# Performance work log

Hardware: AMD Instinct MI355X
Metric: run time of the kernel (lower is better)

The kernel has to match this reference:

```python
import jax, jax.numpy as jnp
import numpy as np

K = 16  # centroids per codebook (4-bit LUT indices, blink-mm convention)


def _im2col(x, kh, kw, stride, pad):
    # x: [B, C, H, W] -> [B, P, C*kh*kw] with channel-major feature ordering
    # (each length-(kh*kw) subvector is one channel's patch, matching the
    #  per-channel codebook layout of the 3x3 AMM conv).
    B, C, H, W = x.shape
    xp = jnp.pad(x, ((0, 0), (0, 0), (pad, pad), (pad, pad)))
    Ho = (H + 2 * pad - kh) // stride + 1
    Wo = (W + 2 * pad - kw) // stride + 1
    cols = [xp[:, :, i:i + stride * Ho:stride, j:j + stride * Wo:stride]
            for i in range(kh) for j in range(kw)]  # fixed small loop (<=9)
    feat = jnp.stack(cols, axis=2)                      # [B, C, kh*kw, Ho, Wo]
    feat = feat.reshape(B, C * kh * kw, Ho, Wo)
    feat = feat.transpose(0, 2, 3, 1).reshape(B, Ho * Wo, C * kh * kw)
    return feat, Ho, Wo


def _amm_conv_bn_act(x, centroids, lut, scale, bias, kernel, stride, pad, relu):
    # Product-quantization approximate matmul conv:
    #  1) im2col, split feature dim D into ncodebooks subspaces of dim dsub
    #  2) nearest-centroid (L2) assignment per subspace -> 4-bit index
    #  3) gather+accumulate precomputed LUT dot products over codebooks
    #  4) folded BatchNorm affine + optional ReLU
    feat, Ho, Wo = _im2col(x, kernel, kernel, stride, pad)
    B, P, D = feat.shape
    ncb, k, dsub = centroids.shape
    xs = feat.reshape(B, P, ncb, dsub)
    dots = jnp.einsum('bpcd,ckd->bpck', xs, centroids)          # [B,P,ncb,K]
    c2 = jnp.sum(centroids * centroids, axis=-1)                # [ncb,K]
    idx = jnp.argmin(c2[None, None] - 2.0 * dots, axis=-1)      # [B,P,ncb]
    onehot = jax.nn.one_hot(idx, k, dtype=x.dtype)              # [B,P,ncb,K]
    out = jnp.einsum('bpck,cko->bpo', onehot, lut)              # LUT accumulate
    out = out * scale + bias                                    # folded BN
    if relu:
        out = jax.nn.relu(out)
    Cout = lut.shape[-1]
    return out.reshape(B, Ho, Wo, Cout).transpose(0, 3, 1, 2)


def setup_inputs() -> dict:
    key = jax.random.key(0)
    ks = jax.random.split(key, 16)
    inplanes, planes, width = 1024, 256, 256
    B, H, W = 32, 14, 14
    d = {}
    d['x'] = jax.random.normal(ks[0], (B, inplanes, H, W), dtype=jnp.float32)
    d['c1_centroids'] = jax.random.normal(ks[1], (inplanes // 4, K, 4), dtype=jnp.float32)
    d['c1_lut'] = jax.random.normal(ks[2], (inplanes // 4, K, width), dtype=jnp.float32) * 0.1
    d['c1_scale'] = jax.random.uniform(ks[3], (width,), dtype=jnp.float32, minval=0.5, maxval=1.5)
    d['c1_bias'] = jax.random.normal(ks[4], (width,), dtype=jnp.float32) * 0.1
    d['c2_centroids'] = jax.random.normal(ks[5], (width, K, 9), dtype=jnp.float32)
    d['c2_lut'] = jax.random.normal(ks[6], (width, K, width), dtype=jnp.float32) * 0.1
    d['c2_scale'] = jax.random.uniform(ks[7], (width,), dtype=jnp.float32, minval=0.5, maxval=1.5)
    d['c2_bias'] = jax.random.normal(ks[8], (width,), dtype=jnp.float32) * 0.1
    d['c3_centroids'] = jax.random.normal(ks[9], (width // 4, K, 4), dtype=jnp.float32)
    d['c3_lut'] = jax.random.normal(ks[10], (width // 4, K, planes * 4), dtype=jnp.float32) * 0.1
    d['c3_scale'] = jax.random.uniform(ks[11], (planes * 4,), dtype=jnp.float32, minval=0.5, maxval=1.5)
    d['c3_bias'] = jax.random.normal(ks[12], (planes * 4,), dtype=jnp.float32) * 0.1
    return d


def reference(x, c1_centroids, c1_lut, c1_scale, c1_bias,
              c2_centroids, c2_lut, c2_scale, c2_bias,
              c3_centroids, c3_lut, c3_scale, c3_bias):
    identity = x
    out = _amm_conv_bn_act(x, c1_centroids, c1_lut, c1_scale, c1_bias,
                           kernel=1, stride=1, pad=0, relu=True)
    out = _amm_conv_bn_act(out, c2_centroids, c2_lut, c2_scale, c2_bias,
                           kernel=3, stride=1, pad=1, relu=True)
    out = _amm_conv_bn_act(out, c3_centroids, c3_lut, c3_scale, c3_bias,
                           kernel=1, stride=1, pad=0, relu=False)
    # QuantizedAdd + QuantizedReLU (float reference math: add then relu)
    return jax.nn.relu(out + identity)
```

## Files before the change

kernel.cpp:

```cpp
#include <hip/hip_runtime.h>
#include <stdint.h>

#define PP 196
#define BP 6272

typedef _Float16 half_t;
typedef half_t half8v __attribute__((ext_vector_type(8)));
typedef half_t half2v __attribute__((ext_vector_type(2)));


template <typename T>
__global__ __launch_bounds__(256) void assign_1x1(
    const T* __restrict__ in, const float* __restrict__ cents,
    uint32_t* __restrict__ idxp, int nchan) {
  __shared__ float  sf[8][16][4];
  __shared__ double sd[8][16][6];
  const int chunk = blockIdx.y;
  const int t = threadIdx.x;
  for (int i = t; i < 512; i += 256) {
    float c = cents[(size_t)chunk * 512 + i];
    int cb = i >> 6, r = i & 63;
    sf[cb][r >> 2][r & 3] = c;
    sd[cb][r >> 2][1 + (r & 3)] = (double)c;
  }
  __syncthreads();
  if (t < 128) {
    int cb = t >> 4, k = t & 15;
    double s = 0.0;
#pragma unroll
    for (int d = 0; d < 4; d++) { double c = sd[cb][k][1 + d]; s += c * c; }
    sd[cb][k][0] = s;
  }
  __syncthreads();
  const int p = blockIdx.x * 256 + t;
  if (p >= BP) return;
  const unsigned b = (unsigned)p / 196u;
  const unsigned pr = (unsigned)p - b * 196u;
  const T* xb = in + ((size_t)b * nchan + chunk * 32) * PP + pr;
  T xr[32];
#pragma unroll
  for (int i = 0; i < 32; i++) xr[i] = xb[(size_t)i * PP];
  float xs2[32];
#pragma unroll
  for (int i = 0; i < 32; i++) xs2[i] = 2.f * (float)xr[i];
  uint32_t word = 0;
#pragma unroll 1
  for (int cb = 0; cb < 8; cb++) {
    float best = 1e30f, sec = 1e30f; int bi = 0;
#pragma unroll
    for (int k = 0; k < 16; k++) {
      const float4 c = *(const float4*)&sf[cb][k][0];
      float dist = c.x * (c.x - xs2[cb * 4 + 0]);
      dist = fmaf(c.y, c.y - xs2[cb * 4 + 1], dist);
      dist = fmaf(c.z, c.z - xs2[cb * 4 + 2], dist);
      dist = fmaf(c.w, c.w - xs2[cb * 4 + 3], dist);
      if (dist < best) { sec = best; best = dist; bi = k; }
      else sec = fminf(sec, dist);
    }
    if (__any(sec - best < 2e-4f)) {
      double xv[4];
#pragma unroll
      for (int d = 0; d < 4; d++) xv[d] = (double)xr[cb * 4 + d];
      double bb = 1e300; int bi64 = 0;
#pragma unroll
      for (int k = 0; k < 16; k++) {
        double dot = 0.0;
#pragma unroll
        for (int d = 0; d < 4; d++) dot = fma(xv[d], sd[cb][k][1 + d], dot);
        double dist = sd[cb][k][0] - 2.0 * dot;
        if (dist < bb) { bb = dist; bi64 = k; }
      }
      bi = bi64;
    }
    word |= (uint32_t)bi << (4 * cb);
  }
  idxp[(size_t)chunk * BP + p] = word;
}

__global__ __launch_bounds__(256) void assign_3x3(
    const double* __restrict__ in, const float* __restrict__ cents,
    uint32_t* __restrict__ idxp) {
  __shared__ float  sf[8][16][12];
  __shared__ double sd[8][16][10];
  const int chunk = blockIdx.y;
  const int c0g = chunk * 8;
  const int t = threadIdx.x;
  for (int i = t; i < 1152; i += 256) {
    int cb = i / 144, r = i - cb * 144;
    int k = r / 9, d = r - k * 9;
    float c = cents[(size_t)(c0g + cb) * 144 + k * 9 + d];
    sf[cb][k][1 + d] = c;
    sd[cb][k][1 + d] = (double)c;
  }
  __syncthreads();
  if (t < 128) {
    int cb = t >> 4, k = t & 15;
    double s = 0.0;
    float s32 = 0.f;
#pragma unroll
    for (int d = 0; d < 9; d++) {
      double c = sd[cb][k][1 + d]; s += c * c;
      float cf = sf[cb][k][1 + d]; s32 += cf * cf;
    }
    sd[cb][k][0] = s;
    sf[cb][k][0] = s32;
  }
  __syncthreads();
  const int p = blockIdx.x * 256 + t;
  if (p >= BP) return;
  const unsigned b = (unsigned)p / 196u;
  const unsigned pr = (unsigned)p - b * 196u;
  const int oh = pr / 14, ow = pr - oh * 14;
  uint32_t word = 0;
#pragma unroll 1
  for (int cb = 0; cb < 8; cb++) {
    const double* base = in + ((size_t)b * 256 + (c0g + cb)) * PP;
    double v64[9]; float v32[9];
#pragma unroll
    for (int r = 0; r < 3; r++) {
#pragma unroll
      for (int cc = 0; cc < 3; cc++) {
        int hh = oh + r - 1, ww = ow + cc - 1;
        bool ok = (hh >= 0) & (hh < 14) & (ww >= 0) & (ww < 14);
        double v = ok ? base[hh * 14 + ww] : 0.0;
        v64[r * 3 + cc] = v;
        v32[r * 3 + cc] = (float)v;
      }
    }
    float best = 1e30f, sec = 1e30f; int bi = 0;
#pragma unroll
    for (int k = 0; k < 16; k++) {
      const float4 cA = *(const float4*)&sf[cb][k][0];
      const float4 cB = *(const float4*)&sf[cb][k][4];
      const float4 cC = *(const float4*)&sf[cb][k][8];
      float dot = v32[0] * cA.y;
      dot = fmaf(v32[1], cA.z, dot);
      dot = fmaf(v32[2], cA.w, dot);
      dot = fmaf(v32[3], cB.x, dot);
      dot = fmaf(v32[4], cB.y, dot);
      dot = fmaf(v32[5], cB.z, dot);
      dot = fmaf(v32[6], cB.w, dot);
      dot = fmaf(v32[7], cC.x, dot);
      dot = fmaf(v32[8], cC.y, dot);
      float dist = fmaf(-2.f, dot, cA.x);
      if (dist < best) { sec = best; best = dist; bi = k; }
      else sec = fminf(sec, dist);
    }
    if (__any(sec - best < 4e-4f)) {
      double bb = 1e300; int bi64 = 0;
#pragma unroll
      for (int k = 0; k < 16; k++) {
        double dot = 0.0;
#pragma unroll
        for (int d = 0; d < 9; d++) dot = fma(v64[d], sd[cb][k][1 + d], dot);
        double dist = sd[cb][k][0] - 2.0 * dot;
        if (dist < bb) { bb = dist; bi64 = k; }
      }
      bi = bi64;
    }
    word |= (uint32_t)bi << (4 * cb);
  }
  idxp[(size_t)chunk * BP + p] = word;
}

template <int NCB, int NOUT, bool RELU, bool FUSE3, typename OutT>
__global__ __launch_bounds__(256) void accum_f64(
    const float* __restrict__ lut, const uint32_t* __restrict__ idxp,
    const float* __restrict__ scale, const float* __restrict__ bias,
    const float* __restrict__ c3cent, uint8_t* __restrict__ i3b,
    OutT* __restrict__ out) {
  __shared__ float s_lut[4096];
  __shared__ float  c3f[4][16][4];
  __shared__ float  c3c2f[4][16];
  __shared__ double c3d[4][16][4];
  __shared__ double c3c2d[4][16];
  const int t = threadIdx.x;
  const int lane = t & 63;
  const int q = t >> 6;
  const int p = blockIdx.x * 64 + lane;
  const int o_base = blockIdx.y * 16;
  if (FUSE3 && t < 64) {
    int cb_l = t >> 4, k = t & 15;
    const float4 cf = *(const float4*)(c3cent + ((size_t)(blockIdx.y * 4 + cb_l)) * 64 + k * 4);
    c3f[cb_l][k][0] = cf.x; c3f[cb_l][k][1] = cf.y;
    c3f[cb_l][k][2] = cf.z; c3f[cb_l][k][3] = cf.w;
    double d0 = (double)cf.x, d1 = (double)cf.y, d2 = (double)cf.z, d3 = (double)cf.w;
    c3d[cb_l][k][0] = d0; c3d[cb_l][k][1] = d1;
    c3d[cb_l][k][2] = d2; c3d[cb_l][k][3] = d3;
    double s = 0.0; s += d0 * d0; s += d1 * d1; s += d2 * d2; s += d3 * d3;
    c3c2d[cb_l][k] = s;
    float s32 = 0.f; s32 += cf.x * cf.x; s32 += cf.y * cf.y;
    s32 += cf.z * cf.z; s32 += cf.w * cf.w;
    c3c2f[cb_l][k] = s32;
  }
  const float* src = lut + ((size_t)(t >> 6) * 16 + ((t >> 2) & 15)) * NOUT
                         + o_base + (t & 3) * 4;
  const int kk = (t >> 2) & 15, qs = t & 3;
  const int sslot = (t >> 6) * 64 + qs * 16 + ((kk & 8) | ((kk + 2 * qs) & 7));
  const int q2 = q * 2;
  double a0 = 0, a1 = 0, a2 = 0, a3 = 0;
  constexpr int NCHUNK = NCB / 16;
  for (int ch = 0; ch < NCHUNK; ch++) {
    __syncthreads();
    uint32_t w0 = idxp[(size_t)(ch * 2) * BP + p];
    uint32_t w1 = idxp[(size_t)(ch * 2 + 1) * BP + p];
    {
      const float* g = src + (size_t)(ch * 256) * NOUT;
#pragma unroll
      for (int j = 0; j < 4; j++) {
        float4 v = *(const float4*)(g + (size_t)(64 * j) * NOUT);
        *(float4*)(s_lut + (sslot + 256 * j) * 4) = v;
      }
    }
    __syncthreads();
    const float* buf = s_lut + q * 64;
#pragma unroll
    for (int j = 0; j < 8; j++) {
      uint32_t w = (j < 4) ? w0 : w1;
      int sh = (j & 3) * 8;
      int i0 = (int)((w >> sh) & 15u);
      int i1 = (int)((w >> (sh + 4)) & 15u);
      int o0 = (i0 & 8) | ((i0 + q2) & 7);
      int o1 = (i1 & 8) | ((i1 + q2) & 7);
      const float4 va = *(const float4*)(buf + (2 * j) * 256 + o0 * 4);
      const float4 vb = *(const float4*)(buf + (2 * j + 1) * 256 + o1 * 4);
      float s0 = va.x + vb.x, s1 = va.y + vb.y;
      float s2 = va.z + vb.z, s3 = va.w + vb.w;
      a0 += (double)s0; a1 += (double)s1; a2 += (double)s2; a3 += (double)s3;
    }
  }
  const unsigned b = (unsigned)p / 196u;
  const unsigned pr = (unsigned)p - b * 196u;
  const int o = o_base + q * 4;
  const float4 sc = *(const float4*)(scale + o);
  const float4 bs = *(const float4*)(bias + o);
  double r0 = a0 * (double)sc.x + (double)bs.x;
  double r1 = a1 * (double)sc.y + (double)bs.y;
  double r2 = a2 * (double)sc.z + (double)bs.z;
  double r3 = a3 * (double)sc.w + (double)bs.w;
  if (RELU) {
    r0 = fmax(r0, 0.0); r1 = fmax(r1, 0.0);
    r2 = fmax(r2, 0.0); r3 = fmax(r3, 0.0);
  }
  if (FUSE3) {
    const int cb_l = q;
    float x0 = (float)r0, x1 = (float)r1, x2 = (float)r2, x3 = (float)r3;
    float best = 1e30f, sec = 1e30f; int bi = 0;
#pragma unroll
    for (int k = 0; k < 16; k++) {
      const float4 c = *(const float4*)&c3f[cb_l][k][0];
      float dot = x0 * c.x;
      dot = fmaf(x1, c.y, dot);
      dot = fmaf(x2, c.z, dot);
      dot = fmaf(x3, c.w, dot);
      float dist = fmaf(-2.f, dot, c3c2f[cb_l][k]);
      if (dist < best) { sec = best; best = dist; bi = k; }
      else sec = fminf(sec, dist);
    }
    if (__any(sec - best < 1e-3f)) {
      double bb = 1e300; int bi64 = 0;
#pragma unroll
      for (int k = 0; k < 16; k++) {
        double dot = 0.0;
        dot = fma(r0, c3d[cb_l][k][0], dot);
        dot = fma(r1, c3d[cb_l][k][1], dot);
        dot = fma(r2, c3d[cb_l][k][2], dot);
        dot = fma(r3, c3d[cb_l][k][3], dot);
        double dist = c3c2d[cb_l][k] - 2.0 * dot;
        if (dist < bb) { bb = dist; bi64 = k; }
      }
      bi = bi64;
    }
    i3b[(size_t)p * 64 + blockIdx.y * 4 + q] = (uint8_t)bi;
  } else {
    OutT* op = out + ((size_t)b * NOUT + o) * PP + pr;
    op[0 * PP] = (OutT)r0; op[1 * PP] = (OutT)r1;
    op[2 * PP] = (OutT)r2; op[3 * PP] = (OutT)r3;
  }
}

__global__ __launch_bounds__(256) void accum3_f16(
    const float* __restrict__ lut, const uint8_t* __restrict__ i3b,
    const float* __restrict__ scale, const float* __restrict__ bias,
    const float* __restrict__ res, float* __restrict__ out) {
  __shared__ half_t s16[16 * 640];
  const int t = threadIdx.x;
  const int lane = t & 63;
  const int wave = t >> 6;
  const int h = wave & 1;
  const int pg = wave >> 1;
  const int p = blockIdx.x * 128 + pg * 64 + lane;
  const int o_base = blockIdx.y * 16;
  const int s0 = t, s1 = t + 256;
  const int cA = s0 >> 5, kA = (s0 >> 1) & 15, hA = s0 & 1;
  const int cB = s1 >> 5, kB = (s1 >> 1) & 15, hB = s1 & 1;
  const size_t cs = (size_t)16 * 16 * 1024;
  constexpr int NCHUNK = 4;
  float acc[8];
#pragma unroll
  for (int i = 0; i < 8; i++) acc[i] = 0.f;
  for (int ch = 0; ch < NCHUNK; ch++) {
    __syncthreads();
    const uint4 iw = *(const uint4*)(i3b + (size_t)p * 64 + ch * 16);
    {
      const float* gA = lut + (size_t)ch * cs + ((size_t)cA * 16 + kA) * 1024 + o_base + hA * 8;
      const float* gB = lut + (size_t)ch * cs + ((size_t)cB * 16 + kB) * 1024 + o_base + hB * 8;
      float4 a0 = *(const float4*)gA;
      float4 a1 = *(const float4*)(gA + 4);
      float4 b0 = *(const float4*)gB;
      float4 b1 = *(const float4*)(gB + 4);
      half8v va, vb;
      va[0] = (half_t)a0.x; va[1] = (half_t)a0.y; va[2] = (half_t)a0.z; va[3] = (half_t)a0.w;
      va[4] = (half_t)a1.x; va[5] = (half_t)a1.y; va[6] = (half_t)a1.z; va[7] = (half_t)a1.w;
      vb[0] = (half_t)b0.x; vb[1] = (half_t)b0.y; vb[2] = (half_t)b0.z; vb[3] = (half_t)b0.w;
      vb[4] = (half_t)b1.x; vb[5] = (half_t)b1.y; vb[6] = (half_t)b1.z; vb[7] = (half_t)b1.w;
      *(half8v*)(s16 + cA * 640 + kA * 40 + hA * 8) = va;
      *(half8v*)(s16 + cB * 640 + kB * 40 + hB * 8) = vb;
    }
    __syncthreads();
#pragma unroll
    for (int grp = 0; grp < 2; grp++) {
      uint32_t wa = grp ? iw.z : iw.x;
      uint32_t wb = grp ? iw.w : iw.y;
      half2v p0 = 0, p1 = 0, p2 = 0, p3 = 0;
#pragma unroll
      for (int j = 0; j < 8; j++) {
        uint32_t w = (j < 4) ? wa : wb;
        int idx = (int)((w >> ((j & 3) * 8)) & 15u);
        int cb_l = grp * 8 + j;
        const half8v v = *(const half8v*)(s16 + cb_l * 640 + idx * 40 + h * 8);
        const half2v* vp = (const half2v*)&v;
        p0 += vp[0]; p1 += vp[1]; p2 += vp[2]; p3 += vp[3];
      }
      acc[0] += (float)p0[0]; acc[1] += (float)p0[1];
      acc[2] += (float)p1[0]; acc[3] += (float)p1[1];
      acc[4] += (float)p2[0]; acc[5] += (float)p2[1];
      acc[6] += (float)p3[0]; acc[7] += (float)p3[1];
    }
  }
  const unsigned b = (unsigned)p / 196u;
  const unsigned pr = (unsigned)p - b * 196u;
  const int o = o_base + h * 8;
  const float* rp = res + ((size_t)b * 1024 + o) * PP + pr;
  float* op = out + ((size_t)b * 1024 + o) * PP + pr;
#pragma unroll
  for (int i = 0; i < 8; i++) {
    float v = acc[i] * scale[o + i] + bias[o + i] + rp[(size_t)i * PP];
    op[(size_t)i * PP] = fmaxf(v, 0.f);
  }
}


extern "C" void kernel_launch(void* const* d_in, const int* in_sizes, int n_in,
                              void* d_out, int out_size, void* d_ws, size_t ws_size,
                              hipStream_t stream) {
  const float* x   = (const float*)d_in[0];
  const float* c1c = (const float*)d_in[1];
  const float* c1l = (const float*)d_in[2];
  const float* c1s = (const float*)d_in[3];
  const float* c1b = (const float*)d_in[4];
  const float* c2c = (const float*)d_in[5];
  const float* c2l = (const float*)d_in[6];
  const float* c2s = (const float*)d_in[7];
  const float* c2b = (const float*)d_in[8];
  const float* c3c = (const float*)d_in[9];
  const float* c3l = (const float*)d_in[10];
  const float* c3s = (const float*)d_in[11];
  const float* c3b = (const float*)d_in[12];

  const size_t sz_i1  = (size_t)32 * BP * 4;
  const size_t sz_i2  = (size_t)32 * BP * 4;
  const size_t sz_i3b = (size_t)BP * 64;
  const size_t sz_o64 = (size_t)BP * 256 * 8;

  char* w = (char*)d_ws;
  uint32_t* i1 = (uint32_t*)w; w += sz_i1;
  uint32_t* i2 = (uint32_t*)w; w += sz_i2;
  uint8_t* i3b = (uint8_t*)w;  w += sz_i3b;
  double* out1;
  if (ws_size >= (size_t)(w - (char*)d_ws) + sz_o64) {
    out1 = (double*)w;
  } else {
    out1 = (double*)d_out;
  }

  const dim3 blkA(256), blkC(256);
  assign_1x1<float><<<dim3(25, 32), blkA, 0, stream>>>(x, c1c, i1, 1024);
  accum_f64<256, 256, true, false, double><<<dim3(98, 16), blkC, 0, stream>>>(
      c1l, i1, c1s, c1b, nullptr, nullptr, out1);
  assign_3x3<<<dim3(25, 32), blkA, 0, stream>>>(out1, c2c, i2);
  accum_f64<256, 256, true, true, double><<<dim3(98, 16), blkC, 0, stream>>>(
      c2l, i2, c2s, c2b, c3c, i3b, nullptr);
  accum3_f16<<<dim3(49, 64), blkC, 0, stream>>>(
      c3l, i3b, c3s, c3b, x, (float*)d_out);
}
```

Baseline: 242.1 us.

## Use XOR LUT swizzle, chunk-major index layout, and coalesced LUT staging

The LUT-accumulate kernel replaces its add-and-mask bank swizzle with a plain XOR and processes four codebooks per unrolled step, adding them pairwise before the double accumulation. The stage-3 index bytes are now written chunk-major (16 bytes per pixel per chunk), so the final accumulate kernel reads each chunk's indices as a contiguous uint4 stream. That kernel also stages the LUT into shared memory with four float4 loads per thread, with neighbouring threads reading adjacent columns, instead of two strided 8-float loads. The aim is cheaper address arithmetic, fewer bank conflicts and better-coalesced global traffic. The float summation order changes slightly.

```diff
diff --git a/kernel.cpp b/kernel.cpp
--- a/kernel.cpp
+++ b/kernel.cpp
@@ -6,6 +6,7 @@
 
 typedef _Float16 half_t;
 typedef half_t half8v __attribute__((ext_vector_type(8)));
+typedef half_t half4v __attribute__((ext_vector_type(4)));
 typedef half_t half2v __attribute__((ext_vector_type(2)));
 
 
@@ -196,7 +197,7 @@
   const float* src = lut + ((size_t)(t >> 6) * 16 + ((t >> 2) & 15)) * NOUT
                          + o_base + (t & 3) * 4;
   const int kk = (t >> 2) & 15, qs = t & 3;
-  const int sslot = (t >> 6) * 64 + qs * 16 + ((kk & 8) | ((kk + 2 * qs) & 7));
+  const int sslot = (t >> 6) * 64 + qs * 16 + (kk ^ (2 * qs));
   const int q2 = q * 2;
   double a0 = 0, a1 = 0, a2 = 0, a3 = 0;
   constexpr int NCHUNK = NCB / 16;
@@ -215,17 +216,21 @@
     __syncthreads();
     const float* buf = s_lut + q * 64;
 #pragma unroll
-    for (int j = 0; j < 8; j++) {
-      uint32_t w = (j < 4) ? w0 : w1;
-      int sh = (j & 3) * 8;
+    for (int jq = 0; jq < 4; jq++) {
+      uint32_t w = (jq < 2) ? w0 : w1;
+      int sh = (jq & 1) * 16;
       int i0 = (int)((w >> sh) & 15u);
       int i1 = (int)((w >> (sh + 4)) & 15u);
-      int o0 = (i0 & 8) | ((i0 + q2) & 7);
-      int o1 = (i1 & 8) | ((i1 + q2) & 7);
-      const float4 va = *(const float4*)(buf + (2 * j) * 256 + o0 * 4);
-      const float4 vb = *(const float4*)(buf + (2 * j + 1) * 256 + o1 * 4);
-      float s0 = va.x + vb.x, s1 = va.y + vb.y;
-      float s2 = va.z + vb.z, s3 = va.w + vb.w;
+      int i2 = (int)((w >> (sh + 8)) & 15u);
+      int i3 = (int)((w >> (sh + 12)) & 15u);
+      const float4 va = *(const float4*)(buf + (4 * jq)     * 256 + (i0 ^ q2) * 4);
+      const float4 vb = *(const float4*)(buf + (4 * jq + 1) * 256 + (i1 ^ q2) * 4);
+      const float4 vc = *(const float4*)(buf + (4 * jq + 2) * 256 + (i2 ^ q2) * 4);
+      const float4 vd = *(const float4*)(buf + (4 * jq + 3) * 256 + (i3 ^ q2) * 4);
+      float s0 = (va.x + vb.x) + (vc.x + vd.x);
+      float s1 = (va.y + vb.y) + (vc.y + vd.y);
+      float s2 = (va.z + vb.z) + (vc.z + vd.z);
+      float s3 = (va.w + vb.w) + (vc.w + vd.w);
       a0 += (double)s0; a1 += (double)s1; a2 += (double)s2; a3 += (double)s3;
     }
   }
@@ -271,7 +276,8 @@
       }
       bi = bi64;
     }
-    i3b[(size_t)p * 64 + blockIdx.y * 4 + q] = (uint8_t)bi;
+    i3b[((size_t)(blockIdx.y >> 2) * BP + p) * 16 + (blockIdx.y & 3) * 4 + q] =
+        (uint8_t)bi;
   } else {
     OutT* op = out + ((size_t)b * NOUT + o) * PP + pr;
     op[0 * PP] = (OutT)r0; op[1 * PP] = (OutT)r1;
@@ -291,9 +297,7 @@
   const int pg = wave >> 1;
   const int p = blockIdx.x * 128 + pg * 64 + lane;
   const int o_base = blockIdx.y * 16;
-  const int s0 = t, s1 = t + 256;
-  const int cA = s0 >> 5, kA = (s0 >> 1) & 15, hA = s0 & 1;
-  const int cB = s1 >> 5, kB = (s1 >> 1) & 15, hB = s1 & 1;
+  const int rs = t >> 2, cg = t & 3;
   const size_t cs = (size_t)16 * 16 * 1024;
   constexpr int NCHUNK = 4;
   float acc[8];
@@ -301,21 +305,18 @@
   for (int i = 0; i < 8; i++) acc[i] = 0.f;
   for (int ch = 0; ch < NCHUNK; ch++) {
     __syncthreads();
-    const uint4 iw = *(const uint4*)(i3b + (size_t)p * 64 + ch * 16);
+    const uint4 iw = *(const uint4*)(i3b + ((size_t)ch * BP + p) * 16);
     {
-      const float* gA = lut + (size_t)ch * cs + ((size_t)cA * 16 + kA) * 1024 + o_base + hA * 8;
-      const float* gB = lut + (size_t)ch * cs + ((size_t)cB * 16 + kB) * 1024 + o_base + hB * 8;
-      float4 a0 = *(const float4*)gA;
-      float4 a1 = *(const float4*)(gA + 4);
-      float4 b0 = *(const float4*)gB;
-      float4 b1 = *(const float4*)(gB + 4);
-      half8v va, vb;
-      va[0] = (half_t)a0.x; va[1] = (half_t)a0.y; va[2] = (half_t)a0.z; va[3] = (half_t)a0.w;
-      va[4] = (half_t)a1.x; va[5] = (half_t)a1.y; va[6] = (half_t)a1.z; va[7] = (half_t)a1.w;
-      vb[0] = (half_t)b0.x; vb[1] = (half_t)b0.y; vb[2] = (half_t)b0.z; vb[3] = (half_t)b0.w;
-      vb[4] = (half_t)b1.x; vb[5] = (half_t)b1.y; vb[6] = (half_t)b1.z; vb[7] = (half_t)b1.w;
-      *(half8v*)(s16 + cA * 640 + kA * 40 + hA * 8) = va;
-      *(half8v*)(s16 + cB * 640 + kB * 40 + hB * 8) = vb;
+#pragma unroll
+      for (int j = 0; j < 4; j++) {
+        const int r = rs + 64 * j;
+        const float4 v = *(const float4*)(lut + (size_t)ch * cs +
+                                          (size_t)r * 1024 + o_base + cg * 4);
+        half4v hv;
+        hv[0] = (half_t)v.x; hv[1] = (half_t)v.y;
+        hv[2] = (half_t)v.z; hv[3] = (half_t)v.w;
+        *(half4v*)(s16 + (r >> 4) * 640 + (r & 15) * 40 + cg * 4) = hv;
+      }
     }
     __syncthreads();
 #pragma unroll
```

After: 226.7 us. 1.07x faster.
